# Kernel tuning notes

Hardware: AMD Instinct MI355X
Metric: run time of the kernel (lower is better)

The kernel has to match this reference:

```python
import jax, jax.numpy as jnp
import numpy as np
from jax import lax

D = 33            # n_vertices
NEG_SLOPE = 0.2   # LeakyReLU slope
EPS_IN = 1e-5     # InstanceNorm eps


def _block(x, w, b, gamma, beta):
    # Conv2d(k=3, stride=2, pad=1) -> LeakyReLU(0.2) -> optional InstanceNorm2d(affine)
    y = lax.conv_general_dilated(x, w, (2, 2), [(1, 1), (1, 1)],
                                 dimension_numbers=('NCHW', 'OIHW', 'NCHW'))
    y = y + b[None, :, None, None]
    y = jnp.where(y >= 0, y, NEG_SLOPE * y)
    if gamma is not None:
        mu = jnp.mean(y, (2, 3), keepdims=True)
        var = jnp.var(y, (2, 3), keepdims=True)
        y = (y - mu) * lax.rsqrt(var + EPS_IN) * gamma[None, :, None, None] + beta[None, :, None, None]
    return y


def _backbone(lq, w1, b1, g1, be1, w2, b2, g2, be2, w3, b3, g3, be3,
              w4, b4, g4, be4, w5, b5):
    B = lq.shape[0]
    # F.interpolate(..., 256, bilinear, align_corners=False) == half-pixel linear, no antialias
    x = jax.image.resize(lq, (B, 3, 256, 256), method='linear', antialias=False)
    x = _block(x, w1, b1, g1, be1)   # [B,16,128,128]
    x = _block(x, w2, b2, g2, be2)   # [B,32,64,64]
    x = _block(x, w3, b3, g3, be3)   # [B,64,32,32]
    x = _block(x, w4, b4, g4, be4)   # [B,128,16,16]
    x = _block(x, w5, b5, None, None)  # [B,128,8,8]; Dropout is identity in eval
    # AdaptiveAvgPool2d(2) on 8x8 -> mean over 4x4 blocks
    x = x.reshape(B, 128, 2, 4, 2, 4).mean((3, 5))  # [B,128,2,2]
    return x.reshape(B, -1)  # [B,512]


def _trilerp(lut, r, g, b):
    # lut [3,D,D,D]; r,g,b [N] in [0, D-1]; align_corners=True + border padding
    i0 = jnp.clip(jnp.floor(r).astype(jnp.int32), 0, D - 2)
    j0 = jnp.clip(jnp.floor(g).astype(jnp.int32), 0, D - 2)
    k0 = jnp.clip(jnp.floor(b).astype(jnp.int32), 0, D - 2)
    fr, fg, fb = r - i0, g - j0, b - k0

    def c(di, dj, dk):
        return lut[:, i0 + di, j0 + dj, k0 + dk]  # [3,N]

    return (c(0, 0, 0) * (1 - fr) * (1 - fg) * (1 - fb)
            + c(0, 0, 1) * (1 - fr) * (1 - fg) * fb
            + c(0, 1, 0) * (1 - fr) * fg * (1 - fb)
            + c(0, 1, 1) * (1 - fr) * fg * fb
            + c(1, 0, 0) * fr * (1 - fg) * (1 - fb)
            + c(1, 0, 1) * fr * (1 - fg) * fb
            + c(1, 1, 0) * fr * fg * (1 - fb)
            + c(1, 1, 1) * fr * fg * fb)


def _ailut_transform(img, luts, vertices):
    # img [B,3,H,W] in [0,1]; luts [B,3,D,D,D]; vertices [B,3,D] sorted in [0,1]
    B, C, H, W = img.shape
    p = img.reshape(B, C, -1)  # [B,3,N]
    # per-(b,c) searchsorted(right=True)
    idx = jax.vmap(jax.vmap(lambda v, x: jnp.searchsorted(v, x, side='right')))(vertices, p)
    idx = jnp.clip(idx, 1, D - 1)
    v_lo = jnp.take_along_axis(vertices, idx - 1, axis=-1)
    v_hi = jnp.take_along_axis(vertices, idx, axis=-1)
    frac = (p - v_lo) / (v_hi - v_lo + 1e-8)
    coord = (idx - 1).astype(img.dtype) + frac        # [B,3,N] in [0, D-1]
    coord = jnp.clip(coord, 0.0, D - 1.0)             # border padding
    # torch grid layout (blue->W, green->H, red->D); LUT axes are (red, green, blue)
    sampled = jax.vmap(_trilerp)(luts, coord[:, 0], coord[:, 1], coord[:, 2])  # [B,3,N]
    return sampled.reshape(B, C, H, W)


def _forward(lq, w1, b1, g1, be1, w2, b2, g2, be2, w3, b3, g3, be3,
             w4, b4, g4, be4, w5, b5, lw, lb, bw, aw, ab):
    B = lq.shape[0]
    codes = _backbone(lq, w1, b1, g1, be1, w2, b2, g2, be2, w3, b3, g3, be3,
                      w4, b4, g4, be4, w5, b5)          # [B,512]
    # LUTGenerator
    weights = codes @ lw.T + lb                          # [B,3]
    luts = (weights @ bw.T).reshape(B, 3, D, D, D)       # [B,3,D,D,D]
    # AdaInt
    intervals = (codes @ aw.T + ab).reshape(B, 3, D - 1)
    intervals = jax.nn.softmax(intervals, axis=-1)
    vertices = jnp.pad(jnp.cumsum(intervals, axis=-1), ((0, 0), (0, 0), (1, 0)))  # [B,3,D]
    outs = jnp.clip(_ailut_transform(lq, luts, vertices), 0.0, 1.0)
    return outs, weights, vertices


def setup_inputs() -> dict:
    key = jax.random.key(0)
    ks = jax.random.split(key, 16)
    B = 4
    lq = jax.random.uniform(ks[0], (B, 3, 1024, 1024), jnp.float32)

    def cw(k, o, i):
        return jax.random.normal(k, (o, i, 3, 3), jnp.float32) * (1.0 / np.sqrt(i * 9))

    w1 = cw(ks[1], 16, 3);   b1 = jnp.zeros(16);  g1 = jnp.ones(16);  be1 = jnp.zeros(16)
    w2 = cw(ks[2], 32, 16);  b2 = jnp.zeros(32);  g2 = jnp.ones(32);  be2 = jnp.zeros(32)
    w3 = cw(ks[3], 64, 32);  b3 = jnp.zeros(64);  g3 = jnp.ones(64);  be3 = jnp.zeros(64)
    w4 = cw(ks[4], 128, 64); b4 = jnp.zeros(128); g4 = jnp.ones(128); be4 = jnp.zeros(128)
    w5 = cw(ks[5], 128, 128); b5 = jnp.zeros(128)

    lw = jax.random.normal(ks[6], (3, 512), jnp.float32) * 0.02
    lb = jnp.ones(3, jnp.float32)  # init: bias = ones
    # basis LUT bank: rank0 = identity LUT (meshgrid/(D-1), channel-flipped), others small
    grid = jnp.stack(jnp.meshgrid(jnp.arange(D), jnp.arange(D), jnp.arange(D),
                                  indexing='ij'), 0).astype(jnp.float32) / (D - 1)
    identity = grid[::-1].reshape(-1, 1)  # [3*D^3,1]
    bw = jnp.concatenate([identity,
                          jax.random.normal(ks[7], (3 * D ** 3, 2), jnp.float32) * 0.01], axis=1)
    aw = jax.random.normal(ks[8], (96, 512), jnp.float32) * 0.01
    ab = jnp.ones(96, jnp.float32)  # init: bias = ones
    return {'lq': lq, 'w1': w1, 'b1': b1, 'g1': g1, 'be1': be1,
            'w2': w2, 'b2': b2, 'g2': g2, 'be2': be2,
            'w3': w3, 'b3': b3, 'g3': g3, 'be3': be3,
            'w4': w4, 'b4': b4, 'g4': g4, 'be4': be4,
            'w5': w5, 'b5': b5, 'lw': lw, 'lb': lb, 'bw': bw, 'aw': aw, 'ab': ab}


def reference(lq, w1, b1, g1, be1, w2, b2, g2, be2, w3, b3, g3, be3,
              w4, b4, g4, be4, w5, b5, lw, lb, bw, aw, ab):
    return _forward(lq, w1, b1, g1, be1, w2, b2, g2, be2, w3, b3, g3, be3,
                    w4, b4, g4, be4, w5, b5, lw, lb, bw, aw, ab)
```

## Files before the change

kernel.cpp:

```cpp
#include <hip/hip_runtime.h>
#include <hip/hip_fp16.h>
#include <math.h>

#define LUT_D 33
#define LUT_D3 35937
#define NEG 0.2f
#define BATCH 4
#define HW_IMG 1048576

template<int IC, int OC, int OH, int OW, int ICCH, bool NORM_IN, bool RESIZE_IN, bool STATS_OUT>
__global__ void __launch_bounds__(256) k_conv2(
    const float* __restrict__ in, const float* __restrict__ part_in,
    const float* __restrict__ g, const float* __restrict__ be, float invN, int ntin,
    const float* __restrict__ w, const float* __restrict__ bias,
    float* __restrict__ out, float* __restrict__ part_out) {
    constexpr int IH = OH * 2, IW = OW * 2;
    constexpr int NCH = IC / ICCH;
    constexpr int TROW = 20, TSZ = 17 * TROW;
    constexpr int NTX = OW / 8, NTY = OH / 8, NOCG = OC / 16;
    constexpr int NT = NTX * NTY;

    __shared__ float sIn[ICCH * TSZ];
    __shared__ float swl[16 * ICCH * 9];
    __shared__ float sNm[NORM_IN ? IC * 2 : 1];

    int id = blockIdx.x;
    int ocg = id % NOCG;  id /= NOCG;
    int tx  = id % NTX;   id /= NTX;
    int ty  = id % NTY;   id /= NTY;
    int b   = id;

    int t    = threadIdx.x;
    int lane = t >> 6;
    int px   = t & 63;
    int py   = px >> 3, pxx = px & 7;
    int oc0  = ocg * 16 + lane * 4;

    if (NORM_IN) {
        constexpr int P = 256 / IC;
        int c = t / P, r = t % P;
        float s1 = 0.f, s2 = 0.f;
        for (int i = r; i < ntin; i += P) {
            const float* pp = part_in + ((size_t)(b * IC + c) * ntin + i) * 2;
            s1 += pp[0]; s2 += pp[1];
        }
        #pragma unroll
        for (int off = P >> 1; off > 0; off >>= 1) {
            s1 += __shfl_down(s1, off, 64);
            s2 += __shfl_down(s2, off, 64);
        }
        if (r == 0) {
            float m   = s1 * invN;
            float var = s2 * invN - m * m;
            float sc  = g[c] * rsqrtf(var + 1e-5f);
            sNm[c * 2]     = sc;
            sNm[c * 2 + 1] = be[c] - m * sc;
        }
        __syncthreads();
    }

    float acc[4];
    #pragma unroll
    for (int j = 0; j < 4; j++) acc[j] = bias[oc0 + j];

    int iy0 = ty * 16 - 1;
    int xbase = tx * 16;

    for (int ch = 0; ch < NCH; ch++) {
        int icc = ch * ICCH;
        if (ch) __syncthreads();

        if (IC == ICCH) {
            const float4* wsrc = (const float4*)(w + (size_t)ocg * 16 * IC * 9);
            for (int i = t; i < 16 * IC * 9 / 4; i += 256) ((float4*)swl)[i] = wsrc[i];
        } else {
            constexpr int WQ = ICCH * 9 / 4;
            for (int i = t; i < 16 * WQ; i += 256) {
                int ol = i / WQ, qi = i % WQ;
                ((float4*)swl)[ol * WQ + qi] =
                    *(const float4*)(w + ((size_t)(ocg * 16 + ol) * IC + icc) * 9 + qi * 4);
            }
        }

        if (RESIZE_IN) {
            for (int q = t; q < ICCH * 17 * 4; q += 256) {
                int ic_l = q / 68;
                int r2   = q % 68;
                int row  = r2 >> 2, quad = r2 & 3;
                int iy = iy0 + row;
                float4 v = {0.f, 0.f, 0.f, 0.f};
                if (iy >= 0 && iy < IH) {
                    const float* lb_ = in + (size_t)(b * IC + icc + ic_l) * HW_IMG
                                          + (size_t)(4 * iy + 1) * 1024;
                    int c0 = (xbase + quad * 4) * 4;
                    const float4* pa = (const float4*)(lb_ + c0);
                    const float4* pb = (const float4*)(lb_ + 1024 + c0);
                    float4 a0 = pa[0], a1 = pa[1], a2 = pa[2], a3 = pa[3];
                    float4 q0 = pb[0], q1 = pb[1], q2 = pb[2], q3 = pb[3];
                    v.x = 0.25f * (a0.y + a0.z + q0.y + q0.z);
                    v.y = 0.25f * (a1.y + a1.z + q1.y + q1.z);
                    v.z = 0.25f * (a2.y + a2.z + q2.y + q2.z);
                    v.w = 0.25f * (a3.y + a3.z + q3.y + q3.z);
                }
                *(float4*)(sIn + ic_l * TSZ + row * TROW + 4 + quad * 4) = v;
            }
            for (int h = t; h < ICCH * 17; h += 256) {
                int ic_l = h / 17, row = h % 17;
                int iy = iy0 + row, ix = xbase - 1;
                float v = 0.f;
                if (iy >= 0 && iy < IH && ix >= 0) {
                    const float* lb_ = in + (size_t)(b * IC + icc + ic_l) * HW_IMG
                                          + (size_t)(4 * iy + 1) * 1024;
                    float4 a = *(const float4*)(lb_ + ix * 4);
                    float4 q0 = *(const float4*)(lb_ + 1024 + ix * 4);
                    v = 0.25f * (a.y + a.z + q0.y + q0.z);
                }
                sIn[ic_l * TSZ + row * TROW + 3] = v;
            }
        } else {
            const float* inb = in + (size_t)(b * IC + icc) * (IH * IW);
            for (int q = t; q < ICCH * 17 * 4; q += 256) {
                int ic_l = q / 68;
                int r2   = q % 68;
                int row  = r2 >> 2, quad = r2 & 3;
                int iy = iy0 + row;
                float4 v = {0.f, 0.f, 0.f, 0.f};
                if (iy >= 0 && iy < IH) {
                    v = *(const float4*)(inb + (size_t)ic_l * (IH * IW)
                                             + (size_t)iy * IW + xbase + quad * 4);
                    if (NORM_IN) {
                        float sc = sNm[(icc + ic_l) * 2], sh = sNm[(icc + ic_l) * 2 + 1];
                        v.x = v.x * sc + sh; v.y = v.y * sc + sh;
                        v.z = v.z * sc + sh; v.w = v.w * sc + sh;
                    }
                }
                *(float4*)(sIn + ic_l * TSZ + row * TROW + 4 + quad * 4) = v;
            }
            for (int h = t; h < ICCH * 17; h += 256) {
                int ic_l = h / 17, row = h % 17;
                int iy = iy0 + row, ix = xbase - 1;
                float v = 0.f;
                if (iy >= 0 && iy < IH && ix >= 0) {
                    v = inb[(size_t)ic_l * (IH * IW) + (size_t)iy * IW + ix];
                    if (NORM_IN) v = v * sNm[(icc + ic_l) * 2] + sNm[(icc + ic_l) * 2 + 1];
                }
                sIn[ic_l * TSZ + row * TROW + 3] = v;
            }
        }
        __syncthreads();

        for (int i2 = 0; i2 < ICCH; i2++) {
            const float* tp = sIn + i2 * TSZ + py * 2 * TROW + pxx * 2 + 3;
            float x0 = tp[0],        x1 = tp[1],        x2 = tp[2];
            float x3 = tp[TROW],     x4 = tp[TROW + 1], x5 = tp[TROW + 2];
            float x6 = tp[2 * TROW], x7 = tp[2 * TROW + 1], x8 = tp[2 * TROW + 2];
            #pragma unroll
            for (int j = 0; j < 4; j++) {
                const float* wp = swl + ((lane * 4 + j) * ICCH + i2) * 9;
                acc[j] = fmaf(x0, wp[0], acc[j]);
                acc[j] = fmaf(x1, wp[1], acc[j]);
                acc[j] = fmaf(x2, wp[2], acc[j]);
                acc[j] = fmaf(x3, wp[3], acc[j]);
                acc[j] = fmaf(x4, wp[4], acc[j]);
                acc[j] = fmaf(x5, wp[5], acc[j]);
                acc[j] = fmaf(x6, wp[6], acc[j]);
                acc[j] = fmaf(x7, wp[7], acc[j]);
                acc[j] = fmaf(x8, wp[8], acc[j]);
            }
        }
    }

    int oy = ty * 8 + py, ox = tx * 8 + pxx;
    int tile = ty * NTX + tx;
    #pragma unroll
    for (int j = 0; j < 4; j++) {
        float a = acc[j];
        a = a >= 0.f ? a : NEG * a;
        out[((size_t)(b * OC + oc0 + j) * OH + oy) * OW + ox] = a;
        if (STATS_OUT) {
            float s1 = a, s2 = a * a;
            for (int off = 32; off > 0; off >>= 1) {
                s1 += __shfl_down(s1, off, 64);
                s2 += __shfl_down(s2, off, 64);
            }
            if (px == 0) {
                size_t pi = ((size_t)(b * OC + oc0 + j) * NT + tile) * 2;
                part_out[pi] = s1; part_out[pi + 1] = s2;
            }
        }
    }
}

__global__ void k_head(const float* __restrict__ f5, const float* __restrict__ lw,
                       const float* __restrict__ lb, const float* __restrict__ aw,
                       const float* __restrict__ ab, float* __restrict__ wt,
                       float* __restrict__ vert, float* __restrict__ gT,
                       float* __restrict__ out_w, float* __restrict__ out_v) {
    int blk = blockIdx.x;
    int t = threadIdx.x;
    if (blk == 12) {
        __shared__ float sc2[2048];
        for (int s = t; s < 2048; s += 64) {
            int b = s >> 9, rest = s & 511, oc = rest >> 2, q = rest & 3;
            int py = (q >> 1) * 4, pxq = (q & 1) * 4;
            const float* p = f5 + (size_t)(b * 128 + oc) * 64;
            float sum = 0.f;
            #pragma unroll
            for (int dy = 0; dy < 4; dy++) {
                float4 v = *(const float4*)(p + (py + dy) * 8 + pxq);
                sum += v.x + v.y + v.z + v.w;
            }
            sc2[s] = sum * (1.f / 16.f);
        }
        __syncthreads();
        if (t < 48) {
            int j = t >> 2, q = t & 3;
            int b = j / 3, jj = j % 3;
            const float4* c4 = (const float4*)(sc2 + b * 512 + q * 128);
            const float4* l4 = (const float4*)(lw + jj * 512 + q * 128);
            float s = 0.f;
            for (int k = 0; k < 32; k++) {
                float4 cv = c4[k], lv = l4[k];
                s += cv.x * lv.x + cv.y * lv.y + cv.z * lv.z + cv.w * lv.w;
            }
            s += __shfl_down(s, 2, 64);
            s += __shfl_down(s, 1, 64);
            if (q == 0) { s += lb[jj]; wt[j] = s; out_w[j] = s; }
        }
        return;
    }
    int b = blk / 3, ch = blk % 3;
    __shared__ float scode[512];
    __shared__ float y[32];
    __shared__ float vsh[33];
    for (int s = t; s < 512; s += 64) {
        int oc = s >> 2, q = s & 3;
        int py = (q >> 1) * 4, pxq = (q & 1) * 4;
        const float* p = f5 + (size_t)(b * 128 + oc) * 64;
        float sum = 0.f;
        #pragma unroll
        for (int dy = 0; dy < 4; dy++) {
            float4 v = *(const float4*)(p + (py + dy) * 8 + pxq);
            sum += v.x + v.y + v.z + v.w;
        }
        scode[s] = sum * (1.f / 16.f);
    }
    __syncthreads();
    {
        int m = t & 31, half = t >> 5;
        const float4* c4 = (const float4*)(scode + half * 256);
        const float4* a4 = (const float4*)(aw + (size_t)(ch * 32 + m) * 512 + half * 256);
        float s = (half == 0) ? ab[ch * 32 + m] : 0.f;
        for (int k = 0; k < 64; k++) {
            float4 cv = c4[k], av = a4[k];
            s += cv.x * av.x + cv.y * av.y + cv.z * av.z + cv.w * av.w;
        }
        s += __shfl_down(s, 32, 64);
        if (half == 0) y[m] = s;
    }
    __syncthreads();
    if (t == 0) {
        float mx = y[0];
        for (int m = 1; m < 32; m++) mx = fmaxf(mx, y[m]);
        float e[32];
        float sum = 0.f;
        for (int m = 0; m < 32; m++) { e[m] = expf(y[m] - mx); sum += e[m]; }
        float inv = 1.f / sum;
        float cum = 0.f;
        float* vb = vert + (b * 3 + ch) * 33;
        float* ob = out_v + (b * 3 + ch) * 33;
        vb[0] = 0.f; ob[0] = 0.f; vsh[0] = 0.f;
        for (int m = 0; m < 32; m++) {
            cum += e[m] * inv;
            vb[m + 1] = cum; ob[m + 1] = cum; vsh[m + 1] = cum;
        }
    }
    __syncthreads();
    float* T = gT + (size_t)(b * 3 + ch) * 1280;
    for (int u = t; u < 256; u += 64) {
        float lo = (float)u * (1.f / 256.f);
        float hi = (float)(u + 1) * (1.f / 256.f);
        int n0 = 0, nin = 0;
        float vs = 2.0f;
        #pragma unroll
        for (int m = 0; m < 33; m++) {
            float vm = vsh[m];
            n0 += (vm <= lo) ? 1 : 0;
            if (vm > lo && vm < hi) { if (nin == 0) vs = vm; nin++; }
        }
        int i0 = n0 < 1 ? 1 : (n0 > 32 ? 32 : n0);
        int i1 = (n0 + 1) < 1 ? 1 : ((n0 + 1) > 32 ? 32 : (n0 + 1));
        float m0 = 1.f / (vsh[i0] - vsh[i0 - 1] + 1e-8f);
        float c0 = (float)(i0 - 1) - vsh[i0 - 1] * m0;
        float m1 = 1.f / (vsh[i1] - vsh[i1 - 1] + 1e-8f);
        float c1 = (float)(i1 - 1) - vsh[i1 - 1] * m1;
        if (nin >= 2) { vs = 2.0f; m0 = __int_as_float(0x7fc00000); c0 = 0.f; }
        T[u * 5]     = vs;
        T[u * 5 + 1] = m0;
        T[u * 5 + 2] = c0;
        T[u * 5 + 3] = m1;
        T[u * 5 + 4] = c1;
    }
}

__global__ void k_cells(const float* __restrict__ bw, const float* __restrict__ wtp,
                        float4* __restrict__ cells) {
    int gid = blockIdx.x * 256 + threadIdx.x;
    if (gid >= BATCH * 32768) return;
    int b = gid >> 15;
    int cell = gid & 32767;
    int k0 = cell & 31, j0 = (cell >> 5) & 31, i0 = cell >> 10;
    float w0 = wtp[b * 3], w1 = wtp[b * 3 + 1], w2 = wtp[b * 3 + 2];
    int ci[4] = { (i0 * 33 + j0) * 33 + k0,
                  (i0 * 33 + j0 + 1) * 33 + k0,
                  ((i0 + 1) * 33 + j0) * 33 + k0,
                  ((i0 + 1) * 33 + j0 + 1) * 33 + k0 };
    float h[24];
    #pragma unroll
    for (int c = 0; c < 4; c++) {
        #pragma unroll
        for (int kk = 0; kk < 2; kk++) {
            int id2 = ci[c] + kk;
            #pragma unroll
            for (int pl = 0; pl < 3; pl++) {
                const float* p = bw + ((size_t)(pl * LUT_D3 + id2)) * 3;
                h[c * 6 + kk * 3 + pl] = p[0] * w0 + p[1] * w1 + p[2] * w2;
            }
        }
    }
    union { float4 f4[3]; __half hh[24]; } u;
    #pragma unroll
    for (int i = 0; i < 24; i++) u.hh[i] = __float2half_rn(h[i]);
    float4* dst = cells + (size_t)gid * 4;
    dst[0] = u.f4[0]; dst[1] = u.f4[1]; dst[2] = u.f4[2];
}

__device__ __forceinline__ void searchL5(const float* __restrict__ T,
                                         const float* __restrict__ v33,
                                         float x, int& i0, float& f) {
    int u = (int)(x * 256.f);
    u = u < 0 ? 0 : (u > 255 ? 255 : u);
    const float* e = T + u * 5;
    float vs = e[0];
    float coord = (x < vs) ? fmaf(e[1], x, e[2]) : fmaf(e[3], x, e[4]);
    if (!(coord == coord)) {
        int lo = 0, hi = LUT_D;
        while (lo < hi) { int mid = (lo + hi) >> 1; if (v33[mid] <= x) lo = mid + 1; else hi = mid; }
        int idx = lo < 1 ? 1 : (lo > LUT_D - 1 ? LUT_D - 1 : lo);
        float vl = v33[idx - 1], vh = v33[idx];
        coord = (float)(idx - 1) + (x - vl) / (vh - vl + 1e-8f);
    }
    coord = fminf(fmaxf(coord, 0.f), (float)(LUT_D - 1));
    i0 = (int)coord;
    if (i0 > LUT_D - 2) i0 = LUT_D - 2;
    f = coord - (float)i0;
}

__device__ __forceinline__ void decode_lerp3(float wa, float wb, float wc, float fb,
                                             float& rv, float& gv, float& bv) {
    union { float f; __half2 h; } u0, u1, u2;
    u0.f = wa; u1.f = wb; u2.f = wc;
    float2 a = __half22float2(u0.h);
    float2 b = __half22float2(u1.h);
    float2 c = __half22float2(u2.h);
    rv = fmaf(fb, b.y - a.x, a.x);
    gv = fmaf(fb, c.x - a.y, a.y);
    bv = fmaf(fb, c.y - b.x, b.x);
}

__global__ void __launch_bounds__(256) k_transform(const float* __restrict__ lq,
                                                   const float4* __restrict__ cells,
                                                   const float* __restrict__ vert,
                                                   const float* __restrict__ gT,
                                                   float* __restrict__ out) {
    int orig = blockIdx.x;
    int xcd  = orig & 7;
    int bimg = xcd >> 1;
    int blk  = ((orig >> 3) << 1) | (xcd & 1);

    __shared__ float sT[3840];
    __shared__ float sv[100];

    int p0 = blk * 1024 + threadIdx.x * 4;
    const float* lr = lq + (size_t)bimg * 3 * HW_IMG + p0;
    float4 r4 = *(const float4*)(lr);
    float4 g4 = *(const float4*)(lr + HW_IMG);
    float4 b4 = *(const float4*)(lr + 2 * HW_IMG);

    for (int i = threadIdx.x; i < 3840; i += 256) sT[i] = gT[bimg * 3840 + i];
    if (threadIdx.x < 99) sv[threadIdx.x] = vert[bimg * 99 + threadIdx.x];
    __syncthreads();

    float rr[4] = {r4.x, r4.y, r4.z, r4.w};
    float gg[4] = {g4.x, g4.y, g4.z, g4.w};
    float bb[4] = {b4.x, b4.y, b4.z, b4.w};

    int cidx[4];
    float fra[4], fga[4], fba[4];
    #pragma unroll
    for (int i = 0; i < 4; i++) {
        int i0, j0, k0;
        searchL5(sT,        sv,      rr[i], i0, fra[i]);
        searchL5(sT + 1280, sv + 33, gg[i], j0, fga[i]);
        searchL5(sT + 2560, sv + 66, bb[i], k0, fba[i]);
        cidx[i] = ((i0 * 32 + j0) << 5) + k0;
    }
    float4 c0[4], c1[4], c2[4];
    #pragma unroll
    for (int i = 0; i < 4; i++) {
        const float4* p = cells + (((size_t)(bimg << 15) + cidx[i]) << 2);
        c0[i] = p[0]; c1[i] = p[1]; c2[i] = p[2];
    }
    float ro[4], go[4], bo[4];
    #pragma unroll
    for (int i = 0; i < 4; i++) {
        float fb = fba[i];
        float r00, g00, b00, r01, g01, b01, r10, g10, b10, r11, g11, b11;
        decode_lerp3(c0[i].x, c0[i].y, c0[i].z, fb, r00, g00, b00);
        decode_lerp3(c0[i].w, c1[i].x, c1[i].y, fb, r01, g01, b01);
        decode_lerp3(c1[i].z, c1[i].w, c2[i].x, fb, r10, g10, b10);
        decode_lerp3(c2[i].y, c2[i].z, c2[i].w, fb, r11, g11, b11);
        float fr = fra[i], fg = fga[i];
        float w00 = (1.f - fr) * (1.f - fg), w01 = (1.f - fr) * fg;
        float w10 = fr * (1.f - fg),         w11 = fr * fg;
        float rx = r00 * w00 + r01 * w01 + r10 * w10 + r11 * w11;
        float ry = g00 * w00 + g01 * w01 + g10 * w10 + g11 * w11;
        float rz = b00 * w00 + b01 * w01 + b10 * w10 + b11 * w11;
        ro[i] = fminf(fmaxf(rx, 0.f), 1.f);
        go[i] = fminf(fmaxf(ry, 0.f), 1.f);
        bo[i] = fminf(fmaxf(rz, 0.f), 1.f);
    }
    float* op = out + (size_t)bimg * 3 * HW_IMG + p0;
    float4 o0 = {ro[0], ro[1], ro[2], ro[3]};
    float4 o1 = {go[0], go[1], go[2], go[3]};
    float4 o2 = {bo[0], bo[1], bo[2], bo[3]};
    *(float4*)(op) = o0;
    *(float4*)(op + HW_IMG) = o1;
    *(float4*)(op + 2 * HW_IMG) = o2;
}

extern "C" void kernel_launch(void* const* d_in, const int* in_sizes, int n_in,
                              void* d_out, int out_size, void* d_ws, size_t ws_size,
                              hipStream_t stream) {
    const float* lq  = (const float*)d_in[0];
    const float* w1  = (const float*)d_in[1];
    const float* b1  = (const float*)d_in[2];
    const float* g1  = (const float*)d_in[3];
    const float* be1 = (const float*)d_in[4];
    const float* w2  = (const float*)d_in[5];
    const float* b2  = (const float*)d_in[6];
    const float* g2  = (const float*)d_in[7];
    const float* be2 = (const float*)d_in[8];
    const float* w3  = (const float*)d_in[9];
    const float* b3  = (const float*)d_in[10];
    const float* g3  = (const float*)d_in[11];
    const float* be3 = (const float*)d_in[12];
    const float* w4  = (const float*)d_in[13];
    const float* b4  = (const float*)d_in[14];
    const float* g4  = (const float*)d_in[15];
    const float* be4 = (const float*)d_in[16];
    const float* w5  = (const float*)d_in[17];
    const float* b5  = (const float*)d_in[18];
    const float* lw  = (const float*)d_in[19];
    const float* lb  = (const float*)d_in[20];
    const float* bw  = (const float*)d_in[21];
    const float* aw  = (const float*)d_in[22];
    const float* ab  = (const float*)d_in[23];

    float* ws    = (float*)d_ws;
    float* cells = ws;
    float* f1    = ws;
    float* f2    = f1 + 1048576;
    float* f3    = f2 + 524288;
    float* f4    = f3 + 262144;
    float* f5    = f4 + 131072;
    float* tail  = ws + 2097152;
    float* wt    = tail;
    float* vert  = wt + 12;
    float* part1 = vert + 396;
    float* part2 = part1 + 32768;
    float* part3 = part2 + 16384;
    float* part4 = part3 + 8192;
    float* gT    = part4 + 4096;

    float* outs  = (float*)d_out;
    float* out_w = outs + (size_t)BATCH * 3 * HW_IMG;
    float* out_v = out_w + 12;

    k_conv2<3, 16, 128, 128, 3, false, true, true><<<1024, 256, 0, stream>>>(
        lq, nullptr, nullptr, nullptr, 0.f, 0, w1, b1, f1, part1);
    k_conv2<16, 32, 64, 64, 16, true, false, true><<<512, 256, 0, stream>>>(
        f1, part1, g1, be1, 1.f / 16384.f, 256, w2, b2, f2, part2);
    k_conv2<32, 64, 32, 32, 32, true, false, true><<<256, 256, 0, stream>>>(
        f2, part2, g2, be2, 1.f / 4096.f, 64, w3, b3, f3, part3);
    k_conv2<64, 128, 16, 16, 32, true, false, true><<<128, 256, 0, stream>>>(
        f3, part3, g3, be3, 1.f / 1024.f, 16, w4, b4, f4, part4);
    k_conv2<128, 128, 8, 8, 32, true, false, false><<<32, 256, 0, stream>>>(
        f4, part4, g4, be4, 1.f / 256.f, 4, w5, b5, f5, nullptr);
    k_head<<<13, 64, 0, stream>>>(f5, lw, lb, aw, ab, wt, vert, gT, out_w, out_v);
    k_cells<<<512, 256, 0, stream>>>(bw, wt, (float4*)cells);
    k_transform<<<BATCH * 1024, 256, 0, stream>>>(lq, (const float4*)cells, vert, gT, outs);
}
```

Baseline: 326.8 us.

## Split input channels across blocks for deep convs and widen transform per thread

The last two conv layers, which launched very few blocks, now split the input channels across blocks (4 and 8 ways). Each block writes partial sums to a scratch buffer, and a new combine kernel adds them, applies bias and LeakyReLU, and computes per-wave InstanceNorm statistics. This is meant to fill more compute units on the small layers, at the cost of extra partial-sum traffic and two additional launches. Separately, the LUT transform kernel now handles 8 pixels per thread instead of 4 and launches half as many blocks, trading occupancy for more memory-level parallelism per thread.

Result: faster. 289.3 us (-11.5%).

```diff
diff --git a/kernel.cpp b/kernel.cpp
--- a/kernel.cpp
+++ b/kernel.cpp
@@ -8,27 +8,30 @@
 #define BATCH 4
 #define HW_IMG 1048576
 
-template<int IC, int OC, int OH, int OW, int ICCH, bool NORM_IN, bool RESIZE_IN, bool STATS_OUT>
+template<int IC, int OC, int OH, int OW, int NSPLIT, bool NORM_IN, bool RESIZE_IN, bool STATS_OUT>
 __global__ void __launch_bounds__(256) k_conv2(
     const float* __restrict__ in, const float* __restrict__ part_in,
     const float* __restrict__ g, const float* __restrict__ be, float invN, int ntin,
     const float* __restrict__ w, const float* __restrict__ bias,
     float* __restrict__ out, float* __restrict__ part_out) {
     constexpr int IH = OH * 2, IW = OW * 2;
-    constexpr int NCH = IC / ICCH;
+    constexpr int ICB = IC / NSPLIT;
     constexpr int TROW = 20, TSZ = 17 * TROW;
     constexpr int NTX = OW / 8, NTY = OH / 8, NOCG = OC / 16;
     constexpr int NT = NTX * NTY;
-
-    __shared__ float sIn[ICCH * TSZ];
-    __shared__ float swl[16 * ICCH * 9];
+    constexpr int PX = OH * OW;
+
+    __shared__ float sIn[ICB * TSZ];
+    __shared__ float swl[16 * ICB * 9];
     __shared__ float sNm[NORM_IN ? IC * 2 : 1];
 
     int id = blockIdx.x;
-    int ocg = id % NOCG;  id /= NOCG;
-    int tx  = id % NTX;   id /= NTX;
-    int ty  = id % NTY;   id /= NTY;
-    int b   = id;
+    int ocg   = id % NOCG;   id /= NOCG;
+    int icc_i = id % NSPLIT; id /= NSPLIT;
+    int tx    = id % NTX;    id /= NTX;
+    int ty    = id % NTY;    id /= NTY;
+    int b     = id;
+    int icc   = icc_i * ICB;
 
     int t    = threadIdx.x;
     int lane = t >> 6;
@@ -56,137 +59,165 @@
             sNm[c * 2]     = sc;
             sNm[c * 2 + 1] = be[c] - m * sc;
         }
-        __syncthreads();
-    }
-
-    float acc[4];
-    #pragma unroll
-    for (int j = 0; j < 4; j++) acc[j] = bias[oc0 + j];
+    }
+
+    if (IC == ICB) {
+        const float4* wsrc = (const float4*)(w + (size_t)ocg * 16 * IC * 9);
+        for (int i = t; i < 16 * IC * 9 / 4; i += 256) ((float4*)swl)[i] = wsrc[i];
+    } else {
+        constexpr int WQ = ICB * 9 / 4;
+        for (int i = t; i < 16 * WQ; i += 256) {
+            int ol = i / WQ, qi = i % WQ;
+            ((float4*)swl)[ol * WQ + qi] =
+                *(const float4*)(w + ((size_t)(ocg * 16 + ol) * IC + icc) * 9 + qi * 4);
+        }
+    }
+    if (NORM_IN) __syncthreads();
 
     int iy0 = ty * 16 - 1;
     int xbase = tx * 16;
-
-    for (int ch = 0; ch < NCH; ch++) {
-        int icc = ch * ICCH;
-        if (ch) __syncthreads();
-
-        if (IC == ICCH) {
-            const float4* wsrc = (const float4*)(w + (size_t)ocg * 16 * IC * 9);
-            for (int i = t; i < 16 * IC * 9 / 4; i += 256) ((float4*)swl)[i] = wsrc[i];
-        } else {
-            constexpr int WQ = ICCH * 9 / 4;
-            for (int i = t; i < 16 * WQ; i += 256) {
-                int ol = i / WQ, qi = i % WQ;
-                ((float4*)swl)[ol * WQ + qi] =
-                    *(const float4*)(w + ((size_t)(ocg * 16 + ol) * IC + icc) * 9 + qi * 4);
-            }
-        }
-
-        if (RESIZE_IN) {
-            for (int q = t; q < ICCH * 17 * 4; q += 256) {
-                int ic_l = q / 68;
-                int r2   = q % 68;
-                int row  = r2 >> 2, quad = r2 & 3;
-                int iy = iy0 + row;
-                float4 v = {0.f, 0.f, 0.f, 0.f};
-                if (iy >= 0 && iy < IH) {
-                    const float* lb_ = in + (size_t)(b * IC + icc + ic_l) * HW_IMG
-                                          + (size_t)(4 * iy + 1) * 1024;
-                    int c0 = (xbase + quad * 4) * 4;
-                    const float4* pa = (const float4*)(lb_ + c0);
-                    const float4* pb = (const float4*)(lb_ + 1024 + c0);
-                    float4 a0 = pa[0], a1 = pa[1], a2 = pa[2], a3 = pa[3];
-                    float4 q0 = pb[0], q1 = pb[1], q2 = pb[2], q3 = pb[3];
-                    v.x = 0.25f * (a0.y + a0.z + q0.y + q0.z);
-                    v.y = 0.25f * (a1.y + a1.z + q1.y + q1.z);
-                    v.z = 0.25f * (a2.y + a2.z + q2.y + q2.z);
-                    v.w = 0.25f * (a3.y + a3.z + q3.y + q3.z);
+    if (RESIZE_IN) {
+        for (int q = t; q < ICB * 17 * 4; q += 256) {
+            int ic_l = q / 68;
+            int r2   = q % 68;
+            int row  = r2 >> 2, quad = r2 & 3;
+            int iy = iy0 + row;
+            float4 v = {0.f, 0.f, 0.f, 0.f};
+            if (iy >= 0 && iy < IH) {
+                const float* lb_ = in + (size_t)(b * IC + icc + ic_l) * HW_IMG
+                                      + (size_t)(4 * iy + 1) * 1024;
+                int c0 = (xbase + quad * 4) * 4;
+                const float4* pa = (const float4*)(lb_ + c0);
+                const float4* pb = (const float4*)(lb_ + 1024 + c0);
+                float4 a0 = pa[0], a1 = pa[1], a2 = pa[2], a3 = pa[3];
+                float4 q0 = pb[0], q1 = pb[1], q2 = pb[2], q3 = pb[3];
+                v.x = 0.25f * (a0.y + a0.z + q0.y + q0.z);
+                v.y = 0.25f * (a1.y + a1.z + q1.y + q1.z);
+                v.z = 0.25f * (a2.y + a2.z + q2.y + q2.z);
+                v.w = 0.25f * (a3.y + a3.z + q3.y + q3.z);
+            }
+            *(float4*)(sIn + ic_l * TSZ + row * TROW + 4 + quad * 4) = v;
+        }
+        for (int h = t; h < ICB * 17; h += 256) {
+            int ic_l = h / 17, row = h % 17;
+            int iy = iy0 + row, ix = xbase - 1;
+            float v = 0.f;
+            if (iy >= 0 && iy < IH && ix >= 0) {
+                const float* lb_ = in + (size_t)(b * IC + icc + ic_l) * HW_IMG
+                                      + (size_t)(4 * iy + 1) * 1024;
+                float4 a = *(const float4*)(lb_ + ix * 4);
+                float4 q0 = *(const float4*)(lb_ + 1024 + ix * 4);
+                v = 0.25f * (a.y + a.z + q0.y + q0.z);
+            }
+            sIn[ic_l * TSZ + row * TROW + 3] = v;
+        }
+    } else {
+        const float* inb = in + (size_t)(b * IC + icc) * (IH * IW);
+        for (int q = t; q < ICB * 17 * 4; q += 256) {
+            int ic_l = q / 68;
+            int r2   = q % 68;
+            int row  = r2 >> 2, quad = r2 & 3;
+            int iy = iy0 + row;
+            float4 v = {0.f, 0.f, 0.f, 0.f};
+            if (iy >= 0 && iy < IH) {
+                v = *(const float4*)(inb + (size_t)ic_l * (IH * IW)
+                                         + (size_t)iy * IW + xbase + quad * 4);
+                if (NORM_IN) {
+                    float sc = sNm[(icc + ic_l) * 2], sh = sNm[(icc + ic_l) * 2 + 1];
+                    v.x = v.x * sc + sh; v.y = v.y * sc + sh;
+                    v.z = v.z * sc + sh; v.w = v.w * sc + sh;
                 }
-                *(float4*)(sIn + ic_l * TSZ + row * TROW + 4 + quad * 4) = v;
-            }
-            for (int h = t; h < ICCH * 17; h += 256) {
-                int ic_l = h / 17, row = h % 17;
-                int iy = iy0 + row, ix = xbase - 1;
-                float v = 0.f;
-                if (iy >= 0 && iy < IH && ix >= 0) {
-                    const float* lb_ = in + (size_t)(b * IC + icc + ic_l) * HW_IMG
-                                          + (size_t)(4 * iy + 1) * 1024;
-                    float4 a = *(const float4*)(lb_ + ix * 4);
-                    float4 q0 = *(const float4*)(lb_ + 1024 + ix * 4);
-                    v = 0.25f * (a.y + a.z + q0.y + q0.z);
+            }
+            *(float4*)(sIn + ic_l * TSZ + row * TROW + 4 + quad * 4) = v;
+        }
+        for (int h = t; h < ICB * 17; h += 256) {
+            int ic_l = h / 17, row = h % 17;
+            int iy = iy0 + row, ix = xbase - 1;
+            float v = 0.f;
+            if (iy >= 0 && iy < IH && ix >= 0) {
+                v = inb[(size_t)ic_l * (IH * IW) + (size_t)iy * IW + ix];
+                if (NORM_IN) v = v * sNm[(icc + ic_l) * 2] + sNm[(icc + ic_l) * 2 + 1];
+            }
+            sIn[ic_l * TSZ + row * TROW + 3] = v;
+        }
+    }
+    __syncthreads();
+
+    float acc[4];
+    #pragma unroll
+    for (int j = 0; j < 4; j++) acc[j] = (NSPLIT == 1) ? bias[oc0 + j] : 0.f;
+
+    for (int i2 = 0; i2 < ICB; i2++) {
+        const float* tp = sIn + i2 * TSZ + py * 2 * TROW + pxx * 2 + 3;
+        float x0 = tp[0],        x1 = tp[1],        x2 = tp[2];
+        float x3 = tp[TROW],     x4 = tp[TROW + 1], x5 = tp[TROW + 2];
+        float x6 = tp[2 * TROW], x7 = tp[2 * TROW + 1], x8 = tp[2 * TROW + 2];
+        #pragma unroll
+        for (int j = 0; j < 4; j++) {
+            const float* wp = swl + ((lane * 4 + j) * ICB + i2) * 9;
+            acc[j] = fmaf(x0, wp[0], acc[j]);
+            acc[j] = fmaf(x1, wp[1], acc[j]);
+            acc[j] = fmaf(x2, wp[2], acc[j]);
+            acc[j] = fmaf(x3, wp[3], acc[j]);
+            acc[j] = fmaf(x4, wp[4], acc[j]);
+            acc[j] = fmaf(x5, wp[5], acc[j]);
+            acc[j] = fmaf(x6, wp[6], acc[j]);
+            acc[j] = fmaf(x7, wp[7], acc[j]);
+            acc[j] = fmaf(x8, wp[8], acc[j]);
+        }
+    }
+
+    int oy = ty * 8 + py, ox = tx * 8 + pxx;
+    if (NSPLIT == 1) {
+        int tile = ty * NTX + tx;
+        #pragma unroll
+        for (int j = 0; j < 4; j++) {
+            float a = acc[j];
+            a = a >= 0.f ? a : NEG * a;
+            out[((size_t)(b * OC + oc0 + j) * OH + oy) * OW + ox] = a;
+            if (STATS_OUT) {
+                float s1 = a, s2 = a * a;
+                for (int off = 32; off > 0; off >>= 1) {
+                    s1 += __shfl_down(s1, off, 64);
+                    s2 += __shfl_down(s2, off, 64);
                 }
-                sIn[ic_l * TSZ + row * TROW + 3] = v;
-            }
-        } else {
-            const float* inb = in + (size_t)(b * IC + icc) * (IH * IW);
-            for (int q = t; q < ICCH * 17 * 4; q += 256) {
-                int ic_l = q / 68;
-                int r2   = q % 68;
-                int row  = r2 >> 2, quad = r2 & 3;
-                int iy = iy0 + row;
-                float4 v = {0.f, 0.f, 0.f, 0.f};
-                if (iy >= 0 && iy < IH) {
-                    v = *(const float4*)(inb + (size_t)ic_l * (IH * IW)
-                                             + (size_t)iy * IW + xbase + quad * 4);
-                    if (NORM_IN) {
-                        float sc = sNm[(icc + ic_l) * 2], sh = sNm[(icc + ic_l) * 2 + 1];
-                        v.x = v.x * sc + sh; v.y = v.y * sc + sh;
-                        v.z = v.z * sc + sh; v.w = v.w * sc + sh;
-                    }
+                if (px == 0) {
+                    size_t pi = ((size_t)(b * OC + oc0 + j) * NT + tile) * 2;
+                    part_out[pi] = s1; part_out[pi + 1] = s2;
                 }
-                *(float4*)(sIn + ic_l * TSZ + row * TROW + 4 + quad * 4) = v;
-            }
-            for (int h = t; h < ICCH * 17; h += 256) {
-                int ic_l = h / 17, row = h % 17;
-                int iy = iy0 + row, ix = xbase - 1;
-                float v = 0.f;
-                if (iy >= 0 && iy < IH && ix >= 0) {
-                    v = inb[(size_t)ic_l * (IH * IW) + (size_t)iy * IW + ix];
-                    if (NORM_IN) v = v * sNm[(icc + ic_l) * 2] + sNm[(icc + ic_l) * 2 + 1];
-                }
-                sIn[ic_l * TSZ + row * TROW + 3] = v;
-            }
-        }
-        __syncthreads();
-
-        for (int i2 = 0; i2 < ICCH; i2++) {
-            const float* tp = sIn + i2 * TSZ + py * 2 * TROW + pxx * 2 + 3;
-            float x0 = tp[0],        x1 = tp[1],        x2 = tp[2];
-            float x3 = tp[TROW],     x4 = tp[TROW + 1], x5 = tp[TROW + 2];
-            float x6 = tp[2 * TROW], x7 = tp[2 * TROW + 1], x8 = tp[2 * TROW + 2];
-            #pragma unroll
-            for (int j = 0; j < 4; j++) {
-                const float* wp = swl + ((lane * 4 + j) * ICCH + i2) * 9;
-                acc[j] = fmaf(x0, wp[0], acc[j]);
-                acc[j] = fmaf(x1, wp[1], acc[j]);
-                acc[j] = fmaf(x2, wp[2], acc[j]);
-                acc[j] = fmaf(x3, wp[3], acc[j]);
-                acc[j] = fmaf(x4, wp[4], acc[j]);
-                acc[j] = fmaf(x5, wp[5], acc[j]);
-                acc[j] = fmaf(x6, wp[6], acc[j]);
-                acc[j] = fmaf(x7, wp[7], acc[j]);
-                acc[j] = fmaf(x8, wp[8], acc[j]);
-            }
-        }
-    }
-
-    int oy = ty * 8 + py, ox = tx * 8 + pxx;
-    int tile = ty * NTX + tx;
-    #pragma unroll
-    for (int j = 0; j < 4; j++) {
-        float a = acc[j];
-        a = a >= 0.f ? a : NEG * a;
-        out[((size_t)(b * OC + oc0 + j) * OH + oy) * OW + ox] = a;
-        if (STATS_OUT) {
-            float s1 = a, s2 = a * a;
-            for (int off = 32; off > 0; off >>= 1) {
-                s1 += __shfl_down(s1, off, 64);
-                s2 += __shfl_down(s2, off, 64);
-            }
-            if (px == 0) {
-                size_t pi = ((size_t)(b * OC + oc0 + j) * NT + tile) * 2;
-                part_out[pi] = s1; part_out[pi + 1] = s2;
-            }
+            }
+        }
+    } else {
+        #pragma unroll
+        for (int j = 0; j < 4; j++) {
+            part_out[(size_t)icc_i * (BATCH * OC * PX) +
+                     (size_t)(b * OC + oc0 + j) * PX + oy * OW + ox] = acc[j];
+        }
+    }
+}
+
+template<int NSPLIT, int OC, int PX, bool STATS>
+__global__ void k_combine(const float* __restrict__ ps, const float* __restrict__ bias,
+                          float* __restrict__ out, float* __restrict__ spart) {
+    constexpr int TOT = BATCH * OC * PX;
+    int e = blockIdx.x * 256 + threadIdx.x;
+    if (e >= TOT) return;
+    float s = 0.f;
+    #pragma unroll
+    for (int k = 0; k < NSPLIT; k++) s += ps[(size_t)k * TOT + e];
+    int oc = (e / PX) % OC;
+    s += bias[oc];
+    s = s >= 0.f ? s : NEG * s;
+    out[e] = s;
+    if (STATS) {
+        float s1 = s, s2 = s * s;
+        for (int off = 32; off > 0; off >>= 1) {
+            s1 += __shfl_down(s1, off, 64);
+            s2 += __shfl_down(s2, off, 64);
+        }
+        if ((threadIdx.x & 63) == 0) {
+            int widx = e >> 6;
+            spart[widx * 2] = s1; spart[widx * 2 + 1] = s2;
         }
     }
 }
@@ -381,39 +412,42 @@
     __shared__ float sT[3840];
     __shared__ float sv[100];
 
-    int p0 = blk * 1024 + threadIdx.x * 4;
+    int p0 = blk * 2048 + threadIdx.x * 8;
     const float* lr = lq + (size_t)bimg * 3 * HW_IMG + p0;
-    float4 r4 = *(const float4*)(lr);
-    float4 g4 = *(const float4*)(lr + HW_IMG);
-    float4 b4 = *(const float4*)(lr + 2 * HW_IMG);
+    float4 ra = *(const float4*)(lr);
+    float4 rb = *(const float4*)(lr + 4);
+    float4 ga = *(const float4*)(lr + HW_IMG);
+    float4 gb = *(const float4*)(lr + HW_IMG + 4);
+    float4 ba = *(const float4*)(lr + 2 * HW_IMG);
+    float4 bb4 = *(const float4*)(lr + 2 * HW_IMG + 4);
 
     for (int i = threadIdx.x; i < 3840; i += 256) sT[i] = gT[bimg * 3840 + i];
     if (threadIdx.x < 99) sv[threadIdx.x] = vert[bimg * 99 + threadIdx.x];
     __syncthreads();
 
-    float rr[4] = {r4.x, r4.y, r4.z, r4.w};
-    float gg[4] = {g4.x, g4.y, g4.z, g4.w};
-    float bb[4] = {b4.x, b4.y, b4.z, b4.w};
-
-    int cidx[4];
-    float fra[4], fga[4], fba[4];
-    #pragma unroll
-    for (int i = 0; i < 4; i++) {
+    float rr[8] = {ra.x, ra.y, ra.z, ra.w, rb.x, rb.y, rb.z, rb.w};
+    float gg[8] = {ga.x, ga.y, ga.z, ga.w, gb.x, gb.y, gb.z, gb.w};
+    float bb[8] = {ba.x, ba.y, ba.z, ba.w, bb4.x, bb4.y, bb4.z, bb4.w};
+
+    int cidx[8];
+    float fra[8], fga[8], fba[8];
+    #pragma unroll
+    for (int i = 0; i < 8; i++) {
         int i0, j0, k0;
         searchL5(sT,        sv,      rr[i], i0, fra[i]);
         searchL5(sT + 1280, sv + 33, gg[i], j0, fga[i]);
         searchL5(sT + 2560, sv + 66, bb[i], k0, fba[i]);
         cidx[i] = ((i0 * 32 + j0) << 5) + k0;
     }
-    float4 c0[4], c1[4], c2[4];
-    #pragma unroll
-    for (int i = 0; i < 4; i++) {
+    float4 c0[8], c1[8], c2[8];
+    #pragma unroll
+    for (int i = 0; i < 8; i++) {
         const float4* p = cells + (((size_t)(bimg << 15) + cidx[i]) << 2);
         c0[i] = p[0]; c1[i] = p[1]; c2[i] = p[2];
     }
-    float ro[4], go[4], bo[4];
-    #pragma unroll
-    for (int i = 0; i < 4; i++) {
+    float ro[8], go[8], bo[8];
+    #pragma unroll
+    for (int i = 0; i < 8; i++) {
         float fb = fba[i];
         float r00, g00, b00, r01, g01, b01, r10, g10, b10, r11, g11, b11;
         decode_lerp3(c0[i].x, c0[i].y, c0[i].z, fb, r00, g00, b00);
@@ -431,12 +465,12 @@
         bo[i] = fminf(fmaxf(rz, 0.f), 1.f);
     }
     float* op = out + (size_t)bimg * 3 * HW_IMG + p0;
-    float4 o0 = {ro[0], ro[1], ro[2], ro[3]};
-    float4 o1 = {go[0], go[1], go[2], go[3]};
-    float4 o2 = {bo[0], bo[1], bo[2], bo[3]};
-    *(float4*)(op) = o0;
-    *(float4*)(op + HW_IMG) = o1;
-    *(float4*)(op + 2 * HW_IMG) = o2;
+    *(float4*)(op)                  = make_float4(ro[0], ro[1], ro[2], ro[3]);
+    *(float4*)(op + 4)              = make_float4(ro[4], ro[5], ro[6], ro[7]);
+    *(float4*)(op + HW_IMG)         = make_float4(go[0], go[1], go[2], go[3]);
+    *(float4*)(op + HW_IMG + 4)     = make_float4(go[4], go[5], go[6], go[7]);
+    *(float4*)(op + 2 * HW_IMG)     = make_float4(bo[0], bo[1], bo[2], bo[3]);
+    *(float4*)(op + 2 * HW_IMG + 4) = make_float4(bo[4], bo[5], bo[6], bo[7]);
 }
 
 extern "C" void kernel_launch(void* const* d_in, const int* in_sizes, int n_in,
@@ -474,6 +508,8 @@
     float* f3    = f2 + 524288;
     float* f4    = f3 + 262144;
     float* f5    = f4 + 131072;
+    float* psplit4 = f1;
+    float* psplit5 = f1 + 524288;
     float* tail  = ws + 2097152;
     float* wt    = tail;
     float* vert  = wt + 12;
@@ -487,17 +523,19 @@
     float* out_w = outs + (size_t)BATCH * 3 * HW_IMG;
     float* out_v = out_w + 12;
 
-    k_conv2<3, 16, 128, 128, 3, false, true, true><<<1024, 256, 0, stream>>>(
+    k_conv2<3, 16, 128, 128, 1, false, true, true><<<1024, 256, 0, stream>>>(
         lq, nullptr, nullptr, nullptr, 0.f, 0, w1, b1, f1, part1);
-    k_conv2<16, 32, 64, 64, 16, true, false, true><<<512, 256, 0, stream>>>(
+    k_conv2<16, 32, 64, 64, 1, true, false, true><<<512, 256, 0, stream>>>(
         f1, part1, g1, be1, 1.f / 16384.f, 256, w2, b2, f2, part2);
-    k_conv2<32, 64, 32, 32, 32, true, false, true><<<256, 256, 0, stream>>>(
+    k_conv2<32, 64, 32, 32, 1, true, false, true><<<256, 256, 0, stream>>>(
         f2, part2, g2, be2, 1.f / 4096.f, 64, w3, b3, f3, part3);
-    k_conv2<64, 128, 16, 16, 32, true, false, true><<<128, 256, 0, stream>>>(
-        f3, part3, g3, be3, 1.f / 1024.f, 16, w4, b4, f4, part4);
-    k_conv2<128, 128, 8, 8, 32, true, false, false><<<32, 256, 0, stream>>>(
-        f4, part4, g4, be4, 1.f / 256.f, 4, w5, b5, f5, nullptr);
+    k_conv2<64, 128, 16, 16, 4, true, false, false><<<512, 256, 0, stream>>>(
+        f3, part3, g3, be3, 1.f / 1024.f, 16, w4, b4, nullptr, psplit4);
+    k_combine<4, 128, 256, true><<<512, 256, 0, stream>>>(psplit4, b4, f4, part4);
+    k_conv2<128, 128, 8, 8, 8, true, false, false><<<256, 256, 0, stream>>>(
+        f4, part4, g4, be4, 1.f / 256.f, 4, w5, b5, nullptr, psplit5);
+    k_combine<8, 128, 64, false><<<128, 256, 0, stream>>>(psplit5, b5, f5, nullptr);
     k_head<<<13, 64, 0, stream>>>(f5, lw, lb, aw, ab, wt, vert, gT, out_w, out_v);
     k_cells<<<512, 256, 0, stream>>>(bw, wt, (float4*)cells);
-    k_transform<<<BATCH * 1024, 256, 0, stream>>>(lq, (const float4*)cells, vert, gT, outs);
-}
+    k_transform<<<2048, 256, 0, stream>>>(lq, (const float4*)cells, vert, gT, outs);
+}
```
